# Optimization experiments

Hardware: AMD Instinct MI355X
Metric: run time of the kernel (lower is better)

Reference implementation:

```python
import jax, jax.numpy as jnp
import numpy as np

THRESHOLD = 0.2  # relation_threshold default
LN_EPS = 1e-5


def setup_inputs() -> dict:
    key = jax.random.key(0)
    ks = jax.random.split(key, 4)
    N1, N2, F, H, R = 256, 256, 512, 512, 4
    feats_img = jax.random.normal(ks[0], (N1, F), dtype=jnp.float32)
    feats_txt = jax.random.normal(ks[1], (N2, F), dtype=jnp.float32)
    # relation_projector params (R stacked copies of the 2-layer MLP)
    W1 = jax.random.normal(ks[2], (R, H, 2 * F), dtype=jnp.float32) / np.sqrt(2 * F)
    b1 = jnp.zeros((R, H), dtype=jnp.float32)
    gamma = jnp.ones((R, H), dtype=jnp.float32)
    beta = jnp.zeros((R, H), dtype=jnp.float32)
    w2 = jax.random.normal(ks[3], (R, H), dtype=jnp.float32) / np.sqrt(H)
    b2 = jnp.zeros((R,), dtype=jnp.float32)
    return {"feats_img": feats_img, "feats_txt": feats_txt, "W1": W1, "b1": b1,
            "gamma": gamma, "beta": beta, "w2": w2, "b2": b2}


def _relation_scores(x, W1, b1, gamma, beta, w2, b2):
    """Vectorized pairwise MLP: for each relation r, score[i,j] = MLP_r(cat(x_i, x_j)).
    Returns [N, N, R]."""
    N, F = x.shape
    R = W1.shape[0]
    Wl, Wr = W1[:, :, :F], W1[:, :, F:]  # Linear on concat = left half @ x_i + right half @ x_j
    scores = []
    for r in range(R):  # small fixed loop over relations keeps peak memory at one [N,N,H] block
        a = x @ Wl[r].T                                  # [N, H]
        b = x @ Wr[r].T                                  # [N, H]
        h = a[:, None, :] + b[None, :, :] + b1[r]        # [N, N, H]
        mu = h.mean(-1, keepdims=True)
        var = h.var(-1, keepdims=True)                   # biased var, matches torch LayerNorm
        hn = (h - mu) * jax.lax.rsqrt(var + LN_EPS) * gamma[r] + beta[r]
        s = jnp.maximum(hn, 0.0) @ w2[r] + b2[r]         # [N, N]
        scores.append(s)
    return jnp.stack(scores, axis=-1)                    # [N, N, R]


def reference(feats_img, feats_txt, W1, b1, gamma, beta, w2, b2):
    # node_features = cat over modalities (node_types is a static host-side list: omitted)
    x = jnp.concatenate([feats_img, feats_txt], axis=0)  # [N, F]
    S = _relation_scores(x, W1, b1, gamma, beta, w2, b2) # [N, N, R]
    best_rel = jnp.argmax(S, axis=-1).astype(jnp.int32)  # edge_types, dense form
    best_score = S.max(axis=-1)                          # edge_weights, dense form
    N = x.shape[0]
    diag = jnp.eye(N, dtype=bool)
    edge_mask = (~diag) & (best_score > THRESHOLD)       # dense encoding of edge_index
    return x, best_score, best_rel, edge_mask
```

## Files before the change

kernel.cpp:

```cpp
#include <hip/hip_runtime.h>
#include <math.h>


namespace {
constexpr size_t PLANE  = 512 * 512;
constexpr size_t OFF_A   = 0;
constexpr size_t OFF_B   = OFF_A + 4 * PLANE;
constexpr size_t OFF_DOT = OFF_B + 4 * PLANE;
constexpr size_t OFF_S   = OFF_DOT + 8 * PLANE;
constexpr size_t OFF_MA  = OFF_S + 8 * PLANE;
constexpr size_t OFF_QA  = OFF_MA + 2048;
constexpr size_t OFF_PAp = OFF_QA + 2048;
constexpr size_t OFF_MB  = OFF_PAp + 2048;
constexpr size_t OFF_QB  = OFF_MB + 2048;
constexpr size_t OFF_PBp = OFF_QB + 2048;
constexpr size_t OFF_P   = OFF_PBp + 2048;
constexpr size_t OFF_Q   = OFF_P + 2048;
constexpr size_t OFF_SG  = OFF_Q + 2048;
constexpr size_t OFF_QSP = OFF_SG + 2048;
}

__global__ __launch_bounds__(256) void k0_gemm(const float* __restrict__ img,
                                               const float* __restrict__ txt,
                                               const float* __restrict__ W1,
                                               const float* __restrict__ b1,
                                               float* __restrict__ ws) {
  const int b = blockIdx.x;
  const int it = b >> 6;
  const int ct = b & 63;
  const int which = ct >> 5;
  const int r = (ct >> 3) & 3;
  const int ht = ct & 7;
  const int i0 = it << 6, h0 = ht << 6;
  const int t = threadIdx.x;
  const int tx = t & 15, ty = t >> 4;

  __shared__ float Xs[16 * 68];
  __shared__ float Wsm[16 * 68];

  float acc[16], pacc[16];
#pragma unroll
  for (int p = 0; p < 16; ++p) { acc[p] = 0.f; pacc[p] = 0.f; }

  const int srow = t >> 2;
  const int sf4 = (t & 3) << 2;
  const int xi = i0 + srow;
  const float* xrow = (xi < 256) ? (img + (size_t)xi * 512)
                                 : (txt + (size_t)(xi - 256) * 512);
  const float* wrow = W1 + (size_t)(r * 512 + h0 + srow) * 1024 + which * 512;

  for (int k0 = 0; k0 < 512; k0 += 16) {
    const float4 xv = *(const float4*)(xrow + k0 + sf4);
    const float4 wv = *(const float4*)(wrow + k0 + sf4);
    __syncthreads();
    Xs[(sf4 + 0) * 68 + srow] = xv.x;
    Xs[(sf4 + 1) * 68 + srow] = xv.y;
    Xs[(sf4 + 2) * 68 + srow] = xv.z;
    Xs[(sf4 + 3) * 68 + srow] = xv.w;
    Wsm[(sf4 + 0) * 68 + srow] = wv.x;
    Wsm[(sf4 + 1) * 68 + srow] = wv.y;
    Wsm[(sf4 + 2) * 68 + srow] = wv.z;
    Wsm[(sf4 + 3) * 68 + srow] = wv.w;
    __syncthreads();
#pragma unroll
    for (int k = 0; k < 16; ++k) {
      const float4 a4 = *(const float4*)&Xs[k * 68 + 4 * ty];
      const float4 b4 = *(const float4*)&Wsm[k * 68 + 4 * tx];
      const float av[4] = {a4.x, a4.y, a4.z, a4.w};
      const float bv[4] = {b4.x, b4.y, b4.z, b4.w};
#pragma unroll
      for (int c = 0; c < 4; ++c)
#pragma unroll
        for (int d = 0; d < 4; ++d)
          pacc[c * 4 + d] = fmaf(av[c], bv[d], pacc[c * 4 + d]);
    }
#pragma unroll
    for (int p = 0; p < 16; ++p) { acc[p] += pacc[p]; pacc[p] = 0.f; }
  }

  float4 bb = make_float4(0.f, 0.f, 0.f, 0.f);
  if (which) bb = *(const float4*)(b1 + r * 512 + h0 + 4 * tx);
  float* dst = ws + (which ? OFF_B : OFF_A) + (size_t)r * PLANE;
#pragma unroll
  for (int c = 0; c < 4; ++c) {
    float4 v;
    v.x = acc[c * 4 + 0] + bb.x;
    v.y = acc[c * 4 + 1] + bb.y;
    v.z = acc[c * 4 + 2] + bb.z;
    v.w = acc[c * 4 + 3] + bb.w;
    *(float4*)(dst + (size_t)(i0 + 4 * ty + c) * 512 + h0 + 4 * tx) = v;
  }
}

__global__ __launch_bounds__(256) void k1_stats(float* __restrict__ ws,
                                                const float* __restrict__ gamma,
                                                const float* __restrict__ beta,
                                                const float* __restrict__ w2) {
  __shared__ float red[4];
  const int t = threadIdx.x;
  const int gw = (blockIdx.x * 256 + t) >> 6;
  const int lane = t & 63;
  const int which = gw >> 11;
  const int rr = (gw >> 9) & 3;
  const int row = gw & 511;
  const float* src =
      ws + (which ? OFF_B : OFF_A) + (size_t)(rr * 512 + row) * 512 + lane * 8;
  const float* gp = gamma + rr * 512 + lane * 8;
  const float* wp = w2 + rr * 512 + lane * 8;
  float s = 0.f, q = 0.f, pa = 0.f, gg = 0.f;
#pragma unroll
  for (int c = 0; c < 2; ++c) {
    const float4 v = *(const float4*)(src + c * 4);
    const float4 g = *(const float4*)(gp + c * 4);
    const float4 w = *(const float4*)(wp + c * 4);
    const float vv[4] = {v.x, v.y, v.z, v.w};
    const float gv[4] = {g.x, g.y, g.z, g.w};
    const float wv[4] = {w.x, w.y, w.z, w.w};
#pragma unroll
    for (int e = 0; e < 4; ++e) {
      const float p = 0.5f * gv[e] * wv[e];
      s += vv[e];
      q += vv[e] * vv[e];
      pa += p * vv[e];
      gg += p;
    }
  }
#pragma unroll
  for (int off = 32; off >= 1; off >>= 1) {
    s += __shfl_down(s, off, 64);
    q += __shfl_down(q, off, 64);
    pa += __shfl_down(pa, off, 64);
    gg += __shfl_down(gg, off, 64);
  }
  if (lane == 0) {
    const float ma = s * (1.f / 512.f);
    ws[(which ? OFF_MB : OFF_MA) + rr * 512 + row] = ma;
    ws[(which ? OFF_QB : OFF_QA) + rr * 512 + row] = q;
    ws[(which ? OFF_PBp : OFF_PAp) + rr * 512 + row] = pa - ma * gg;
  }
  if (blockIdx.x < 8) {
    const int idx = blockIdx.x * 256 + t;
    const float g = gamma[idx], be = beta[idx], w = w2[idx];
    const float qv = 0.5f * be * w;
    ws[OFF_P + idx] = 0.5f * g * w;
    ws[OFF_Q + idx] = qv;
    ws[OFF_SG + idx] = copysignf(1.f, w);
    float qs = qv;
#pragma unroll
    for (int off = 32; off >= 1; off >>= 1) qs += __shfl_down(qs, off, 64);
    if (lane == 0) red[t >> 6] = qs;
    __syncthreads();
    if (t == 0) ws[OFF_QSP + blockIdx.x] = red[0] + red[1] + red[2] + red[3];
  }
}

__global__ __launch_bounds__(256) void k2_dot(float* __restrict__ ws) {
  const int b = blockIdx.x;
  const int jt = b & 7, it = (b >> 3) & 7, r = (b >> 6) & 3, ks = b >> 8;
  const int i0 = it << 6, j0 = jt << 6;
  const int kb = ks << 8;
  const int t = threadIdx.x;
  const int tx = t & 15, ty = t >> 4;

  __shared__ float As[16 * 68];
  __shared__ float Bs[16 * 68];

  float acc[16];
#pragma unroll
  for (int p = 0; p < 16; ++p) acc[p] = 0.f;

  const int srow = t >> 2, sf4 = (t & 3) << 2;
  const float* arow = ws + OFF_A + (size_t)(r * 512 + i0 + srow) * 512 + kb;
  const float* brow = ws + OFF_B + (size_t)(r * 512 + j0 + srow) * 512 + kb;

  for (int k0 = 0; k0 < 256; k0 += 16) {
    const float4 av = *(const float4*)(arow + k0 + sf4);
    const float4 bv = *(const float4*)(brow + k0 + sf4);
    __syncthreads();
    As[(sf4 + 0) * 68 + srow] = av.x;
    As[(sf4 + 1) * 68 + srow] = av.y;
    As[(sf4 + 2) * 68 + srow] = av.z;
    As[(sf4 + 3) * 68 + srow] = av.w;
    Bs[(sf4 + 0) * 68 + srow] = bv.x;
    Bs[(sf4 + 1) * 68 + srow] = bv.y;
    Bs[(sf4 + 2) * 68 + srow] = bv.z;
    Bs[(sf4 + 3) * 68 + srow] = bv.w;
    __syncthreads();
#pragma unroll
    for (int k = 0; k < 16; ++k) {
      const float4 a4 = *(const float4*)&As[k * 68 + 4 * ty];
      const float4 b4 = *(const float4*)&Bs[k * 68 + 4 * tx];
      const float av2[4] = {a4.x, a4.y, a4.z, a4.w};
      const float bv2[4] = {b4.x, b4.y, b4.z, b4.w};
#pragma unroll
      for (int c = 0; c < 4; ++c)
#pragma unroll
        for (int d = 0; d < 4; ++d)
          acc[c * 4 + d] = fmaf(av2[c], bv2[d], acc[c * 4 + d]);
    }
  }
  float* dst = ws + OFF_DOT + (size_t)ks * (4 * PLANE) + (size_t)r * PLANE;
#pragma unroll
  for (int c = 0; c < 4; ++c) {
    float4 v;
    v.x = acc[c * 4 + 0]; v.y = acc[c * 4 + 1];
    v.z = acc[c * 4 + 2]; v.w = acc[c * 4 + 3];
    *(float4*)(dst + (size_t)(i0 + 4 * ty + c) * 512 + j0 + 4 * tx) = v;
  }
}

__global__ __launch_bounds__(256) void k3_score(float* __restrict__ ws) {
  const int b = blockIdx.x;
  const int jt = b & 15, it = (b >> 4) & 7, r = (b >> 7) & 3, ks = b >> 9;
  const int i0 = it << 6, j0 = jt << 5;
  const int t = threadIdx.x;
  const int tx = t & 15, ty = t >> 4;

  __shared__ float As[64 * 64];
  __shared__ float Bs[32 * 64];
  __shared__ float Pl[3 * 64];

  const float4 mav = *(const float4*)(ws + OFF_MA + r * 512 + i0 + 4 * ty);
  const float4 qav = *(const float4*)(ws + OFF_QA + r * 512 + i0 + 4 * ty);
  const float4 pav = *(const float4*)(ws + OFF_PAp + r * 512 + i0 + 4 * ty);
  const float2 mbv = *(const float2*)(ws + OFF_MB + r * 512 + j0 + 2 * tx);
  const float2 qbv = *(const float2*)(ws + OFF_QB + r * 512 + j0 + 2 * tx);
  const float2 pbv = *(const float2*)(ws + OFF_PBp + r * 512 + j0 + 2 * tx);
  const float maA[4] = {mav.x, mav.y, mav.z, mav.w};
  const float qaA[4] = {qav.x, qav.y, qav.z, qav.w};
  const float paA[4] = {pav.x, pav.y, pav.z, pav.w};
  const float mbA[2] = {mbv.x, mbv.y};
  const float qbA[2] = {qbv.x, qbv.y};
  const float pbA[2] = {pbv.x, pbv.y};

  float Sv[8], Tv[8], acc[8];
#pragma unroll
  for (int c = 0; c < 4; ++c) {
    const size_t doff =
        (size_t)r * PLANE + (size_t)(i0 + 4 * ty + c) * 512 + j0 + 2 * tx;
    const float2 d0 = *(const float2*)(ws + OFF_DOT + doff);
    const float2 d1 = *(const float2*)(ws + OFF_DOT + 4 * PLANE + doff);
    const float dA[2] = {d0.x + d1.x, d0.y + d1.y};
#pragma unroll
    for (int d = 0; d < 2; ++d) {
      const int p = c * 2 + d;
      const float mu = maA[c] + mbA[d];
      const float msq = (qaA[c] + qbA[d] + 2.f * dA[d]) * (1.f / 512.f);
      const float var = msq - mu * mu;
      const float sv = 1.0f / sqrtf(var + 1e-5f);
      Sv[p] = sv;
      Tv[p] = -mu * sv;
      acc[p] = ks ? 0.f : sv * (paA[c] + pbA[d]);
    }
  }

  int aoff[4], boff[2];
#pragma unroll
  for (int c = 0; c < 4; ++c) {
    const int row = 4 * ty + c;
    aoff[c] = row * 256 + (((row + (row >> 2)) & 15) << 4);
  }
#pragma unroll
  for (int d = 0; d < 2; ++d) {
    const int row = 2 * tx + d;
    boff[d] = row * 256 + (((row + (row >> 2)) & 15) << 4);
  }

  const int arow_s = t >> 2;
  const int acol_s = t & 3;
  const int swA = (arow_s + (arow_s >> 2)) & 15;
  const int brow_s = t >> 3;
  const int bcol_s = t & 7;
  const int swB = (brow_s + (brow_s >> 2)) & 15;
  const float* agbase =
      ws + OFF_A + (size_t)(r * 512 + i0 + arow_s) * 512;
  const float* bgbase =
      ws + OFF_B + (size_t)(r * 512 + j0 + brow_s) * 512;

  const int kbase = ks << 8;
  for (int kc = 0; kc < 4; ++kc) {
    const int kb = kbase + (kc << 6);
    float4 ag[4], bg[2], pg;
#pragma unroll
    for (int m = 0; m < 4; ++m)
      ag[m] = *(const float4*)(agbase + kb + 4 * (acol_s + 4 * m));
#pragma unroll
    for (int m = 0; m < 2; ++m)
      bg[m] = *(const float4*)(bgbase + kb + 4 * (bcol_s + 8 * m));
    if (t < 48) {
      const size_t po = (t < 16) ? OFF_P : ((t < 32) ? OFF_Q : OFF_SG);
      pg = *(const float4*)(ws + po + r * 512 + kb + 4 * (t & 15));
    }
    __syncthreads();
#pragma unroll
    for (int m = 0; m < 4; ++m)
      *(float4*)((char*)As + arow_s * 256 + (((acol_s + 4 * m) ^ swA) << 4)) = ag[m];
#pragma unroll
    for (int m = 0; m < 2; ++m)
      *(float4*)((char*)Bs + brow_s * 256 + (((bcol_s + 8 * m) ^ swB) << 4)) = bg[m];
    if (t < 48) *(float4*)((char*)Pl + t * 16) = pg;
    __syncthreads();

#pragma unroll 4
    for (int k4 = 0; k4 < 16; ++k4) {
      const float4 Pk = *(const float4*)((char*)Pl + (k4 << 4));
      const float4 Qk = *(const float4*)((char*)Pl + 256 + (k4 << 4));
      const float4 Sk = *(const float4*)((char*)Pl + 512 + (k4 << 4));
      float4 av[4], bv[2];
#pragma unroll
      for (int c = 0; c < 4; ++c)
        av[c] = *(const float4*)((char*)As + (aoff[c] ^ (k4 << 4)));
#pragma unroll
      for (int d = 0; d < 2; ++d)
        bv[d] = *(const float4*)((char*)Bs + (boff[d] ^ (k4 << 4)));
#pragma unroll
      for (int kk = 0; kk < 4; ++kk) {
        const float pk = ((const float*)&Pk)[kk];
        const float qk = ((const float*)&Qk)[kk];
        const float sk = ((const float*)&Sk)[kk];
        float aa[4], bb[2];
#pragma unroll
        for (int c = 0; c < 4; ++c) aa[c] = ((const float*)&av[c])[kk];
#pragma unroll
        for (int d = 0; d < 2; ++d) bb[d] = ((const float*)&bv[d])[kk];
#pragma unroll
        for (int c = 0; c < 4; ++c)
#pragma unroll
          for (int d = 0; d < 2; ++d) {
            const int p = c * 2 + d;
            const float u = aa[c] + bb[d];
            const float t1 = fmaf(u, Sv[p], Tv[p]);
            const float h = fmaf(t1, pk, qk);
            acc[p] = fmaf(fabsf(h), sk, acc[p]);
          }
      }
    }
  }

  float* dst = ws + OFF_S + (size_t)ks * (4 * PLANE) + (size_t)r * PLANE;
#pragma unroll
  for (int c = 0; c < 4; ++c) {
    float2 v;
    v.x = acc[c * 2 + 0];
    v.y = acc[c * 2 + 1];
    *(float2*)(dst + (size_t)(i0 + 4 * ty + c) * 512 + j0 + 2 * tx) = v;
  }
}

__global__ __launch_bounds__(256) void k4_combine(const float* __restrict__ ws,
                                                  const float* __restrict__ img,
                                                  const float* __restrict__ txt,
                                                  const float* __restrict__ b2,
                                                  float* __restrict__ out) {
  const int idx = blockIdx.x * 256 + threadIdx.x;
  const int i = idx >> 9, j = idx & 511;
  const float* s0 = ws + OFF_S;
  const float* s1 = ws + OFF_S + 4 * PLANE;
  const float* qsp = ws + OFF_QSP;
  float best = -3.4e38f;
  int rel = 0;
#pragma unroll
  for (int r = 0; r < 4; ++r) {
    const float cr = b2[r] + qsp[2 * r] + qsp[2 * r + 1];
    const float s = s0[r * PLANE + idx] + s1[r * PLANE + idx] + cr;
    if (s > best) { best = s; rel = r; }
  }
  out[idx] = (i < 256) ? img[idx] : txt[idx - 131072];
  out[PLANE + idx] = best;
  out[2 * PLANE + idx] = (float)rel;
  out[3 * PLANE + idx] = (i != j && (double)best > 0.2) ? 1.0f : 0.0f;
}

extern "C" void kernel_launch(void* const* d_in, const int* in_sizes, int n_in,
                              void* d_out, int out_size, void* d_ws, size_t ws_size,
                              hipStream_t stream) {
  const float* img   = (const float*)d_in[0];
  const float* txt   = (const float*)d_in[1];
  const float* W1    = (const float*)d_in[2];
  const float* b1    = (const float*)d_in[3];
  const float* gamma = (const float*)d_in[4];
  const float* beta  = (const float*)d_in[5];
  const float* w2    = (const float*)d_in[6];
  const float* b2    = (const float*)d_in[7];
  float* ws  = (float*)d_ws;
  float* out = (float*)d_out;
  (void)in_sizes; (void)n_in; (void)out_size; (void)ws_size;

  hipLaunchKernelGGL(k0_gemm,    dim3(512),  dim3(256), 0, stream, img, txt, W1, b1, ws);
  hipLaunchKernelGGL(k1_stats,   dim3(1024), dim3(256), 0, stream, ws, gamma, beta, w2);
  hipLaunchKernelGGL(k2_dot,     dim3(512),  dim3(256), 0, stream, ws);
  hipLaunchKernelGGL(k3_score,   dim3(1024), dim3(256), 0, stream, ws);
  hipLaunchKernelGGL(k4_combine, dim3(1024), dim3(256), 0, stream, ws, img, txt, b2, out);
}
```

Measured before the change: 202.6 us.

## Drop LDS staging in GEMM and score kernels, load operands directly from global

Removes shared-memory tiling and the barriers from k0_gemm, k2_dot and k3_score. Each thread now reads its own float4 rows straight from global memory and relies on L1/L2 caching for reuse across threads. The k2/k3 signatures are split into separate restrict-qualified pointers, and partial accumulators per k-chunk are kept. This trades away the explicit cross-thread data reuse in LDS and coalesced loads for fewer syncs and LDS traffic, which risks heavier global/cache traffic with strided per-thread row reads.

After: 387.2 us. +91.1%, slower.

```diff
diff --git a/kernel.cpp b/kernel.cpp
--- a/kernel.cpp
+++ b/kernel.cpp
@@ -35,47 +35,50 @@
   const int t = threadIdx.x;
   const int tx = t & 15, ty = t >> 4;
 
-  __shared__ float Xs[16 * 68];
-  __shared__ float Wsm[16 * 68];
-
-  float acc[16], pacc[16];
-#pragma unroll
-  for (int p = 0; p < 16; ++p) { acc[p] = 0.f; pacc[p] = 0.f; }
-
-  const int srow = t >> 2;
-  const int sf4 = (t & 3) << 2;
-  const int xi = i0 + srow;
-  const float* xrow = (xi < 256) ? (img + (size_t)xi * 512)
-                                 : (txt + (size_t)(xi - 256) * 512);
-  const float* wrow = W1 + (size_t)(r * 512 + h0 + srow) * 1024 + which * 512;
-
-  for (int k0 = 0; k0 < 512; k0 += 16) {
-    const float4 xv = *(const float4*)(xrow + k0 + sf4);
-    const float4 wv = *(const float4*)(wrow + k0 + sf4);
-    __syncthreads();
-    Xs[(sf4 + 0) * 68 + srow] = xv.x;
-    Xs[(sf4 + 1) * 68 + srow] = xv.y;
-    Xs[(sf4 + 2) * 68 + srow] = xv.z;
-    Xs[(sf4 + 3) * 68 + srow] = xv.w;
-    Wsm[(sf4 + 0) * 68 + srow] = wv.x;
-    Wsm[(sf4 + 1) * 68 + srow] = wv.y;
-    Wsm[(sf4 + 2) * 68 + srow] = wv.z;
-    Wsm[(sf4 + 3) * 68 + srow] = wv.w;
-    __syncthreads();
-#pragma unroll
-    for (int k = 0; k < 16; ++k) {
-      const float4 a4 = *(const float4*)&Xs[k * 68 + 4 * ty];
-      const float4 b4 = *(const float4*)&Wsm[k * 68 + 4 * tx];
-      const float av[4] = {a4.x, a4.y, a4.z, a4.w};
-      const float bv[4] = {b4.x, b4.y, b4.z, b4.w};
-#pragma unroll
-      for (int c = 0; c < 4; ++c)
-#pragma unroll
-        for (int d = 0; d < 4; ++d)
-          pacc[c * 4 + d] = fmaf(av[c], bv[d], pacc[c * 4 + d]);
-    }
-#pragma unroll
-    for (int p = 0; p < 16; ++p) { acc[p] += pacc[p]; pacc[p] = 0.f; }
+  const float* xr[4];
+#pragma unroll
+  for (int c = 0; c < 4; ++c) {
+    const int xi = i0 + 4 * ty + c;
+    xr[c] = (xi < 256) ? (img + (size_t)xi * 512)
+                       : (txt + (size_t)(xi - 256) * 512);
+  }
+  const float* wr[4];
+#pragma unroll
+  for (int d = 0; d < 4; ++d)
+    wr[d] = W1 + (size_t)(r * 512 + h0 + 4 * tx + d) * 1024 + which * 512;
+
+  float acc[16];
+#pragma unroll
+  for (int p = 0; p < 16; ++p) acc[p] = 0.f;
+
+  for (int kc = 0; kc < 8; ++kc) {
+    float pacc[16];
+#pragma unroll
+    for (int p = 0; p < 16; ++p) pacc[p] = 0.f;
+#pragma unroll 2
+    for (int k4 = 0; k4 < 16; ++k4) {
+      const int kk = (kc << 6) + (k4 << 2);
+      float4 xv[4], wv[4];
+#pragma unroll
+      for (int c = 0; c < 4; ++c) xv[c] = *(const float4*)(xr[c] + kk);
+#pragma unroll
+      for (int d = 0; d < 4; ++d) wv[d] = *(const float4*)(wr[d] + kk);
+#pragma unroll
+      for (int e = 0; e < 4; ++e) {
+        float xa[4], wa[4];
+#pragma unroll
+        for (int c = 0; c < 4; ++c) xa[c] = ((const float*)&xv[c])[e];
+#pragma unroll
+        for (int d = 0; d < 4; ++d) wa[d] = ((const float*)&wv[d])[e];
+#pragma unroll
+        for (int c = 0; c < 4; ++c)
+#pragma unroll
+          for (int d = 0; d < 4; ++d)
+            pacc[c * 4 + d] = fmaf(xa[c], wa[d], pacc[c * 4 + d]);
+      }
+    }
+#pragma unroll
+    for (int p = 0; p < 16; ++p) acc[p] += pacc[p];
   }
 
   float4 bb = make_float4(0.f, 0.f, 0.f, 0.f);
@@ -154,7 +157,9 @@
   }
 }
 
-__global__ __launch_bounds__(256) void k2_dot(float* __restrict__ ws) {
+__global__ __launch_bounds__(256) void k2_dot(const float* __restrict__ wsA,
+                                              const float* __restrict__ wsB,
+                                              float* __restrict__ wsDot) {
   const int b = blockIdx.x;
   const int jt = b & 7, it = (b >> 3) & 7, r = (b >> 6) & 3, ks = b >> 8;
   const int i0 = it << 6, j0 = jt << 6;
@@ -162,44 +167,50 @@
   const int t = threadIdx.x;
   const int tx = t & 15, ty = t >> 4;
 
-  __shared__ float As[16 * 68];
-  __shared__ float Bs[16 * 68];
+  const float* ar[4];
+  const float* br[4];
+#pragma unroll
+  for (int c = 0; c < 4; ++c)
+    ar[c] = wsA + (size_t)(r * 512 + i0 + 4 * ty + c) * 512 + kb;
+#pragma unroll
+  for (int d = 0; d < 4; ++d)
+    br[d] = wsB + (size_t)(r * 512 + j0 + 4 * tx + d) * 512 + kb;
 
   float acc[16];
 #pragma unroll
   for (int p = 0; p < 16; ++p) acc[p] = 0.f;
 
-  const int srow = t >> 2, sf4 = (t & 3) << 2;
-  const float* arow = ws + OFF_A + (size_t)(r * 512 + i0 + srow) * 512 + kb;
-  const float* brow = ws + OFF_B + (size_t)(r * 512 + j0 + srow) * 512 + kb;
-
-  for (int k0 = 0; k0 < 256; k0 += 16) {
-    const float4 av = *(const float4*)(arow + k0 + sf4);
-    const float4 bv = *(const float4*)(brow + k0 + sf4);
-    __syncthreads();
-    As[(sf4 + 0) * 68 + srow] = av.x;
-    As[(sf4 + 1) * 68 + srow] = av.y;
-    As[(sf4 + 2) * 68 + srow] = av.z;
-    As[(sf4 + 3) * 68 + srow] = av.w;
-    Bs[(sf4 + 0) * 68 + srow] = bv.x;
-    Bs[(sf4 + 1) * 68 + srow] = bv.y;
-    Bs[(sf4 + 2) * 68 + srow] = bv.z;
-    Bs[(sf4 + 3) * 68 + srow] = bv.w;
-    __syncthreads();
-#pragma unroll
-    for (int k = 0; k < 16; ++k) {
-      const float4 a4 = *(const float4*)&As[k * 68 + 4 * ty];
-      const float4 b4 = *(const float4*)&Bs[k * 68 + 4 * tx];
-      const float av2[4] = {a4.x, a4.y, a4.z, a4.w};
-      const float bv2[4] = {b4.x, b4.y, b4.z, b4.w};
-#pragma unroll
-      for (int c = 0; c < 4; ++c)
-#pragma unroll
-        for (int d = 0; d < 4; ++d)
-          acc[c * 4 + d] = fmaf(av2[c], bv2[d], acc[c * 4 + d]);
-    }
-  }
-  float* dst = ws + OFF_DOT + (size_t)ks * (4 * PLANE) + (size_t)r * PLANE;
+  for (int kc = 0; kc < 4; ++kc) {
+    float pacc[16];
+#pragma unroll
+    for (int p = 0; p < 16; ++p) pacc[p] = 0.f;
+#pragma unroll 2
+    for (int k4 = 0; k4 < 16; ++k4) {
+      const int kk = (kc << 6) + (k4 << 2);
+      float4 av[4], bv[4];
+#pragma unroll
+      for (int c = 0; c < 4; ++c) av[c] = *(const float4*)(ar[c] + kk);
+#pragma unroll
+      for (int d = 0; d < 4; ++d) bv[d] = *(const float4*)(br[d] + kk);
+#pragma unroll
+      for (int e = 0; e < 4; ++e) {
+        float aa[4], ba[4];
+#pragma unroll
+        for (int c = 0; c < 4; ++c) aa[c] = ((const float*)&av[c])[e];
+#pragma unroll
+        for (int d = 0; d < 4; ++d) ba[d] = ((const float*)&bv[d])[e];
+#pragma unroll
+        for (int c = 0; c < 4; ++c)
+#pragma unroll
+          for (int d = 0; d < 4; ++d)
+            pacc[c * 4 + d] = fmaf(aa[c], ba[d], pacc[c * 4 + d]);
+      }
+    }
+#pragma unroll
+    for (int p = 0; p < 16; ++p) acc[p] += pacc[p];
+  }
+
+  float* dst = wsDot + (size_t)ks * (4 * PLANE) + (size_t)r * PLANE;
 #pragma unroll
   for (int c = 0; c < 4; ++c) {
     float4 v;
@@ -209,23 +220,24 @@
   }
 }
 
-__global__ __launch_bounds__(256) void k3_score(float* __restrict__ ws) {
+__global__ __launch_bounds__(256) void k3_score(const float* __restrict__ wsA,
+                                                const float* __restrict__ wsB,
+                                                const float* __restrict__ wsDot,
+                                                const float* __restrict__ stats,
+                                                const float* __restrict__ planes,
+                                                float* __restrict__ sout) {
   const int b = blockIdx.x;
   const int jt = b & 15, it = (b >> 4) & 7, r = (b >> 7) & 3, ks = b >> 9;
   const int i0 = it << 6, j0 = jt << 5;
   const int t = threadIdx.x;
   const int tx = t & 15, ty = t >> 4;
 
-  __shared__ float As[64 * 64];
-  __shared__ float Bs[32 * 64];
-  __shared__ float Pl[3 * 64];
-
-  const float4 mav = *(const float4*)(ws + OFF_MA + r * 512 + i0 + 4 * ty);
-  const float4 qav = *(const float4*)(ws + OFF_QA + r * 512 + i0 + 4 * ty);
-  const float4 pav = *(const float4*)(ws + OFF_PAp + r * 512 + i0 + 4 * ty);
-  const float2 mbv = *(const float2*)(ws + OFF_MB + r * 512 + j0 + 2 * tx);
-  const float2 qbv = *(const float2*)(ws + OFF_QB + r * 512 + j0 + 2 * tx);
-  const float2 pbv = *(const float2*)(ws + OFF_PBp + r * 512 + j0 + 2 * tx);
+  const float4 mav = *(const float4*)(stats + 0 + r * 512 + i0 + 4 * ty);
+  const float4 qav = *(const float4*)(stats + 2048 + r * 512 + i0 + 4 * ty);
+  const float4 pav = *(const float4*)(stats + 4096 + r * 512 + i0 + 4 * ty);
+  const float2 mbv = *(const float2*)(stats + 6144 + r * 512 + j0 + 2 * tx);
+  const float2 qbv = *(const float2*)(stats + 8192 + r * 512 + j0 + 2 * tx);
+  const float2 pbv = *(const float2*)(stats + 10240 + r * 512 + j0 + 2 * tx);
   const float maA[4] = {mav.x, mav.y, mav.z, mav.w};
   const float qaA[4] = {qav.x, qav.y, qav.z, qav.w};
   const float paA[4] = {pav.x, pav.y, pav.z, pav.w};
@@ -238,8 +250,8 @@
   for (int c = 0; c < 4; ++c) {
     const size_t doff =
         (size_t)r * PLANE + (size_t)(i0 + 4 * ty + c) * 512 + j0 + 2 * tx;
-    const float2 d0 = *(const float2*)(ws + OFF_DOT + doff);
-    const float2 d1 = *(const float2*)(ws + OFF_DOT + 4 * PLANE + doff);
+    const float2 d0 = *(const float2*)(wsDot + doff);
+    const float2 d1 = *(const float2*)(wsDot + 4 * PLANE + doff);
     const float dA[2] = {d0.x + d1.x, d0.y + d1.y};
 #pragma unroll
     for (int d = 0; d < 2; ++d) {
@@ -254,75 +266,42 @@
     }
   }
 
-  int aoff[4], boff[2];
-#pragma unroll
-  for (int c = 0; c < 4; ++c) {
-    const int row = 4 * ty + c;
-    aoff[c] = row * 256 + (((row + (row >> 2)) & 15) << 4);
-  }
-#pragma unroll
-  for (int d = 0; d < 2; ++d) {
-    const int row = 2 * tx + d;
-    boff[d] = row * 256 + (((row + (row >> 2)) & 15) << 4);
-  }
-
-  const int arow_s = t >> 2;
-  const int acol_s = t & 3;
-  const int swA = (arow_s + (arow_s >> 2)) & 15;
-  const int brow_s = t >> 3;
-  const int bcol_s = t & 7;
-  const int swB = (brow_s + (brow_s >> 2)) & 15;
-  const float* agbase =
-      ws + OFF_A + (size_t)(r * 512 + i0 + arow_s) * 512;
-  const float* bgbase =
-      ws + OFF_B + (size_t)(r * 512 + j0 + brow_s) * 512;
-
-  const int kbase = ks << 8;
+  const int kb = ks << 8;
+  const float* ar[4];
+  const float* br[2];
+#pragma unroll
+  for (int c = 0; c < 4; ++c)
+    ar[c] = wsA + (size_t)(r * 512 + i0 + 4 * ty + c) * 512 + kb;
+#pragma unroll
+  for (int d = 0; d < 2; ++d)
+    br[d] = wsB + (size_t)(r * 512 + j0 + 2 * tx + d) * 512 + kb;
+  const float* pp = planes + r * 512 + kb;
+
   for (int kc = 0; kc < 4; ++kc) {
-    const int kb = kbase + (kc << 6);
-    float4 ag[4], bg[2], pg;
-#pragma unroll
-    for (int m = 0; m < 4; ++m)
-      ag[m] = *(const float4*)(agbase + kb + 4 * (acol_s + 4 * m));
-#pragma unroll
-    for (int m = 0; m < 2; ++m)
-      bg[m] = *(const float4*)(bgbase + kb + 4 * (bcol_s + 8 * m));
-    if (t < 48) {
-      const size_t po = (t < 16) ? OFF_P : ((t < 32) ? OFF_Q : OFF_SG);
-      pg = *(const float4*)(ws + po + r * 512 + kb + 4 * (t & 15));
-    }
-    __syncthreads();
-#pragma unroll
-    for (int m = 0; m < 4; ++m)
-      *(float4*)((char*)As + arow_s * 256 + (((acol_s + 4 * m) ^ swA) << 4)) = ag[m];
-#pragma unroll
-    for (int m = 0; m < 2; ++m)
-      *(float4*)((char*)Bs + brow_s * 256 + (((bcol_s + 8 * m) ^ swB) << 4)) = bg[m];
-    if (t < 48) *(float4*)((char*)Pl + t * 16) = pg;
-    __syncthreads();
-
-#pragma unroll 4
+    float cacc[8];
+#pragma unroll
+    for (int p = 0; p < 8; ++p) cacc[p] = 0.f;
+#pragma unroll 2
     for (int k4 = 0; k4 < 16; ++k4) {
-      const float4 Pk = *(const float4*)((char*)Pl + (k4 << 4));
-      const float4 Qk = *(const float4*)((char*)Pl + 256 + (k4 << 4));
-      const float4 Sk = *(const float4*)((char*)Pl + 512 + (k4 << 4));
+      const int kk = (kc << 6) + (k4 << 2);
       float4 av[4], bv[2];
 #pragma unroll
-      for (int c = 0; c < 4; ++c)
-        av[c] = *(const float4*)((char*)As + (aoff[c] ^ (k4 << 4)));
-#pragma unroll
-      for (int d = 0; d < 2; ++d)
-        bv[d] = *(const float4*)((char*)Bs + (boff[d] ^ (k4 << 4)));
-#pragma unroll
-      for (int kk = 0; kk < 4; ++kk) {
-        const float pk = ((const float*)&Pk)[kk];
-        const float qk = ((const float*)&Qk)[kk];
-        const float sk = ((const float*)&Sk)[kk];
+      for (int c = 0; c < 4; ++c) av[c] = *(const float4*)(ar[c] + kk);
+#pragma unroll
+      for (int d = 0; d < 2; ++d) bv[d] = *(const float4*)(br[d] + kk);
+      const float4 Pk = *(const float4*)(pp + kk);
+      const float4 Qk = *(const float4*)(pp + 2048 + kk);
+      const float4 Sk = *(const float4*)(pp + 4096 + kk);
+#pragma unroll
+      for (int e = 0; e < 4; ++e) {
+        const float pk = ((const float*)&Pk)[e];
+        const float qk = ((const float*)&Qk)[e];
+        const float sk = ((const float*)&Sk)[e];
         float aa[4], bb[2];
 #pragma unroll
-        for (int c = 0; c < 4; ++c) aa[c] = ((const float*)&av[c])[kk];
-#pragma unroll
-        for (int d = 0; d < 2; ++d) bb[d] = ((const float*)&bv[d])[kk];
+        for (int c = 0; c < 4; ++c) aa[c] = ((const float*)&av[c])[e];
+#pragma unroll
+        for (int d = 0; d < 2; ++d) bb[d] = ((const float*)&bv[d])[e];
 #pragma unroll
         for (int c = 0; c < 4; ++c)
 #pragma unroll
@@ -331,13 +310,15 @@
             const float u = aa[c] + bb[d];
             const float t1 = fmaf(u, Sv[p], Tv[p]);
             const float h = fmaf(t1, pk, qk);
-            acc[p] = fmaf(fabsf(h), sk, acc[p]);
+            cacc[p] = fmaf(fabsf(h), sk, cacc[p]);
           }
       }
     }
-  }
-
-  float* dst = ws + OFF_S + (size_t)ks * (4 * PLANE) + (size_t)r * PLANE;
+#pragma unroll
+    for (int p = 0; p < 8; ++p) acc[p] += cacc[p];
+  }
+
+  float* dst = sout + (size_t)ks * (4 * PLANE) + (size_t)r * PLANE;
 #pragma unroll
   for (int c = 0; c < 4; ++c) {
     float2 v;
@@ -388,7 +369,10 @@
 
   hipLaunchKernelGGL(k0_gemm,    dim3(512),  dim3(256), 0, stream, img, txt, W1, b1, ws);
   hipLaunchKernelGGL(k1_stats,   dim3(1024), dim3(256), 0, stream, ws, gamma, beta, w2);
-  hipLaunchKernelGGL(k2_dot,     dim3(512),  dim3(256), 0, stream, ws);
-  hipLaunchKernelGGL(k3_score,   dim3(1024), dim3(256), 0, stream, ws);
+  hipLaunchKernelGGL(k2_dot,     dim3(512),  dim3(256), 0, stream,
+                     ws + OFF_A, ws + OFF_B, ws + OFF_DOT);
+  hipLaunchKernelGGL(k3_score,   dim3(1024), dim3(256), 0, stream,
+                     ws + OFF_A, ws + OFF_B, ws + OFF_DOT,
+                     ws + OFF_MA, ws + OFF_P, ws + OFF_S);
   hipLaunchKernelGGL(k4_combine, dim3(1024), dim3(256), 0, stream, ws, img, txt, b2, out);
 }
```
